# Kernel tuning notes

Hardware: AMD Instinct MI355X
Metric: run time of the kernel (lower is better)

The kernel has to match this reference:

```python
import jax, jax.numpy as jnp
import numpy as np

D_MODEL = 768
NUM_HEADS = 12
HEAD_DIM = D_MODEL // NUM_HEADS
LN_EPS = 1e-5
MASK_NEG = -1000000.0


def setup_inputs() -> dict:
    key = jax.random.key(0)
    ks = jax.random.split(key, 10)
    B, L, S = 2, 2048, 2048
    s = 1.0 / np.sqrt(D_MODEL)
    return {
        "q": jax.random.normal(ks[0], (B, L, D_MODEL), jnp.float32),
        "k": jax.random.normal(ks[1], (B, S, D_MODEL), jnp.float32),
        "v": jax.random.normal(ks[2], (B, S, D_MODEL), jnp.float32),
        "attention_mask": jnp.ones((B, S), jnp.int32),
        "Wq": jax.random.normal(ks[3], (D_MODEL, D_MODEL), jnp.float32) * s,
        "Wk": jax.random.normal(ks[4], (D_MODEL, D_MODEL), jnp.float32) * s,
        "Wv": jax.random.normal(ks[5], (D_MODEL, D_MODEL), jnp.float32) * s,
        "W": jax.random.normal(ks[6], (D_MODEL, D_MODEL), jnp.float32) * s,
        "b": jnp.zeros((D_MODEL,), jnp.float32),
        "gamma": jnp.ones((D_MODEL,), jnp.float32),
        "beta": jnp.zeros((D_MODEL,), jnp.float32),
    }


def reference(q, k, v, attention_mask, Wq, Wk, Wv, W, b, gamma, beta):
    B, L, D = q.shape
    S = k.shape[1]
    H, hd = NUM_HEADS, HEAD_DIM
    # projections (torch Linear: x @ W^T), split heads -> (B,H,L,hd)
    Q = (q @ Wq.T).reshape(B, L, H, hd).transpose(0, 2, 1, 3)
    K = (k @ Wk.T).reshape(B, S, H, hd).transpose(0, 2, 1, 3)
    V = (v @ Wv.T).reshape(B, S, H, hd).transpose(0, 2, 1, 3)
    # scores (B,H,L,S) with additive key-padding mask
    scores = jnp.einsum("bhld,bhsd->bhls", Q, K) / np.sqrt(hd)
    mask_score = (1.0 - attention_mask.astype(q.dtype))[:, None, None, :] * MASK_NEG
    att = jax.nn.softmax(scores + mask_score, axis=-1)  # dropout p=0 (eval)
    # attend, merge heads, output projection (with bias)
    O = jnp.einsum("bhls,bhsd->bhld", att, V).transpose(0, 2, 1, 3).reshape(B, L, D)
    O = O @ W.T + b  # state dropout p=0 (eval)
    # residual + LayerNorm
    x = q + O
    mu = jnp.mean(x, axis=-1, keepdims=True)
    var = jnp.mean(jnp.square(x - mu), axis=-1, keepdims=True)
    return (x - mu) * jax.lax.rsqrt(var + LN_EPS) * gamma + beta
```

## Files before the change

kernel.cpp:

```cpp
#include <hip/hip_runtime.h>
#include <hip/hip_bf16.h>
#include <math.h>


typedef unsigned short u16;
typedef unsigned int   u32;
typedef __bf16 bf16x8 __attribute__((ext_vector_type(8)));
typedef float  f32x4  __attribute__((ext_vector_type(4)));

#define DM   768
#define MR   4096
#define WSZ  589824

#define LOG2E 1.44269504089f
#define SM_C  15.0f
#define K1    (0.125f * LOG2E)

__device__ inline u16 bfbits(float f) {
    union { __bf16 b; u16 u; } x; x.b = (__bf16)f; return x.u;
}

__device__ inline uint4 cvt8(const float* src) {
    const float4* p = reinterpret_cast<const float4*>(src);
    float4 a = p[0], b = p[1];
    union { __bf16 h[8]; uint4 v; } u;
    u.h[0] = (__bf16)a.x; u.h[1] = (__bf16)a.y; u.h[2] = (__bf16)a.z; u.h[3] = (__bf16)a.w;
    u.h[4] = (__bf16)b.x; u.h[5] = (__bf16)b.y; u.h[6] = (__bf16)b.z; u.h[7] = (__bf16)b.w;
    return u.v;
}

__device__ inline uint4 cvt8v(float4 a, float4 b) {
    union { __bf16 h[8]; uint4 v; } u;
    u.h[0] = (__bf16)a.x; u.h[1] = (__bf16)a.y; u.h[2] = (__bf16)a.z; u.h[3] = (__bf16)a.w;
    u.h[4] = (__bf16)b.x; u.h[5] = (__bf16)b.y; u.h[6] = (__bf16)b.z; u.h[7] = (__bf16)b.w;
    return u.v;
}

__global__ __launch_bounds__(256) void wcvt(
    const float* __restrict__ w0, const float* __restrict__ w1,
    const float* __restrict__ w2, const float* __restrict__ w3,
    u16* __restrict__ dst)
{
    const float* src = (blockIdx.y == 0) ? w0 : (blockIdx.y == 1) ? w1
                     : (blockIdx.y == 2) ? w2 : w3;
    size_t idx = ((size_t)blockIdx.x * 256 + threadIdx.x) * 8;
    *reinterpret_cast<uint4*>(&dst[(size_t)blockIdx.y * WSZ + idx]) = cvt8(&src[idx]);
}

__global__ __launch_bounds__(256, 2) void gemm_qkv(
    const float* __restrict__ xq, const float* __restrict__ xk, const float* __restrict__ xv,
    const u16* __restrict__ Wb4,
    u16* __restrict__ oq, u16* __restrict__ ok, u16* __restrict__ ov)
{
    const int mode = blockIdx.z;
    const float* X = (mode == 0) ? xq : (mode == 1) ? xk : xv;
    const u16* Wb  = Wb4 + (size_t)mode * WSZ;
    u16* out       = (mode == 0) ? oq : (mode == 1) ? ok : ov;

    __shared__ __attribute__((aligned(16))) u16 As[2][64][72];
    __shared__ __attribute__((aligned(16))) u16 Bs[2][64][72];

    const int tid  = threadIdx.x;
    const int lane = tid & 63;
    const int w    = tid >> 6;
    const int wm   = (w >> 1) * 32;
    const int wn   = (w & 1) * 32;
    const int quad = lane >> 4;
    const int l16  = lane & 15;
    const int tm   = blockIdx.x * 64;
    const int tn   = blockIdx.y * 64;

    const int row0 = tid >> 3,         col0 = (tid & 7) * 8;
    const int row1 = (tid + 256) >> 3, col1 = ((tid + 256) & 7) * 8;

    const float* a0p = &X[(size_t)(tm + row0) * 768 + col0];
    const float* a1p = &X[(size_t)(tm + row1) * 768 + col1];
    const u16*   b0p = &Wb[(size_t)(tn + row0) * 768 + col0];
    const u16*   b1p = &Wb[(size_t)(tn + row1) * 768 + col1];

    f32x4 acc[2][2] = {};

    {
        *reinterpret_cast<uint4*>(&As[0][row0][col0]) = cvt8(a0p);
        *reinterpret_cast<uint4*>(&As[0][row1][col1]) = cvt8(a1p);
        *reinterpret_cast<uint4*>(&Bs[0][row0][col0]) = *reinterpret_cast<const uint4*>(b0p);
        *reinterpret_cast<uint4*>(&Bs[0][row1][col1]) = *reinterpret_cast<const uint4*>(b1p);
    }

    for (int kt = 0; kt < 12; kt++) {
        const int cur = kt & 1;
        __syncthreads();

        float4 af0a, af0b, af1a, af1b; uint4 bt0, bt1;
        if (kt < 11) {
            const int ko = (kt + 1) * 64;
            af0a = *reinterpret_cast<const float4*>(a0p + ko);
            af0b = *reinterpret_cast<const float4*>(a0p + ko + 4);
            af1a = *reinterpret_cast<const float4*>(a1p + ko);
            af1b = *reinterpret_cast<const float4*>(a1p + ko + 4);
            bt0  = *reinterpret_cast<const uint4*>(b0p + ko);
            bt1  = *reinterpret_cast<const uint4*>(b1p + ko);
        }

        #pragma unroll
        for (int kk = 0; kk < 2; kk++) {
            bf16x8 a0 = *reinterpret_cast<const bf16x8*>(&As[cur][wm + l16     ][kk*32 + quad*8]);
            bf16x8 a1 = *reinterpret_cast<const bf16x8*>(&As[cur][wm + 16 + l16][kk*32 + quad*8]);
            bf16x8 b0 = *reinterpret_cast<const bf16x8*>(&Bs[cur][wn + l16     ][kk*32 + quad*8]);
            bf16x8 b1 = *reinterpret_cast<const bf16x8*>(&Bs[cur][wn + 16 + l16][kk*32 + quad*8]);
            acc[0][0] = __builtin_amdgcn_mfma_f32_16x16x32_bf16(a0, b0, acc[0][0], 0, 0, 0);
            acc[0][1] = __builtin_amdgcn_mfma_f32_16x16x32_bf16(a0, b1, acc[0][1], 0, 0, 0);
            acc[1][0] = __builtin_amdgcn_mfma_f32_16x16x32_bf16(a1, b0, acc[1][0], 0, 0, 0);
            acc[1][1] = __builtin_amdgcn_mfma_f32_16x16x32_bf16(a1, b1, acc[1][1], 0, 0, 0);
        }

        if (kt < 11) {
            const int nxt = cur ^ 1;
            *reinterpret_cast<uint4*>(&As[nxt][row0][col0]) = cvt8v(af0a, af0b);
            *reinterpret_cast<uint4*>(&As[nxt][row1][col1]) = cvt8v(af1a, af1b);
            *reinterpret_cast<uint4*>(&Bs[nxt][row0][col0]) = bt0;
            *reinterpret_cast<uint4*>(&Bs[nxt][row1][col1]) = bt1;
        }
    }

    #pragma unroll
    for (int i = 0; i < 2; i++)
        #pragma unroll
        for (int j = 0; j < 2; j++)
            #pragma unroll
            for (int r = 0; r < 4; r++) {
                int gm = tm + wm + i * 16 + quad * 4 + r;
                int gn = tn + wn + j * 16 + l16;
                int b = gm >> 11, l = gm & 2047;
                int h = gn >> 6,  d = gn & 63;
                u16 bv = bfbits(acc[i][j][r]);
                if (mode == 2)
                    out[((size_t)(b * 12 + h) * 64 + d) * 2048 + l] = bv;
                else
                    out[((size_t)(b * 12 + h) * 2048 + l) * 64 + d] = bv;
            }
}

__global__ __launch_bounds__(256, 2) void gemm_out(
    const u16* __restrict__ Oa, const u16* __restrict__ Wb,
    const float* __restrict__ bias, const float* __restrict__ resid,
    float* __restrict__ Xb)
{
    __shared__ __attribute__((aligned(16))) u16 As[2][64][72];
    __shared__ __attribute__((aligned(16))) u16 Bs[2][64][72];

    const int tid  = threadIdx.x;
    const int lane = tid & 63;
    const int w    = tid >> 6;
    const int wm   = (w >> 1) * 32;
    const int wn   = (w & 1) * 32;
    const int quad = lane >> 4;
    const int l16  = lane & 15;
    const int tm   = blockIdx.x * 64;
    const int tn   = blockIdx.y * 64;

    const int row0 = tid >> 3,         col0 = (tid & 7) * 8;
    const int row1 = (tid + 256) >> 3, col1 = ((tid + 256) & 7) * 8;

    const u16* a0p = &Oa[(size_t)(tm + row0) * 768 + col0];
    const u16* a1p = &Oa[(size_t)(tm + row1) * 768 + col1];
    const u16* b0p = &Wb[(size_t)(tn + row0) * 768 + col0];
    const u16* b1p = &Wb[(size_t)(tn + row1) * 768 + col1];

    f32x4 acc[2][2] = {};

    {
        *reinterpret_cast<uint4*>(&As[0][row0][col0]) = *reinterpret_cast<const uint4*>(a0p);
        *reinterpret_cast<uint4*>(&As[0][row1][col1]) = *reinterpret_cast<const uint4*>(a1p);
        *reinterpret_cast<uint4*>(&Bs[0][row0][col0]) = *reinterpret_cast<const uint4*>(b0p);
        *reinterpret_cast<uint4*>(&Bs[0][row1][col1]) = *reinterpret_cast<const uint4*>(b1p);
    }

    for (int kt = 0; kt < 12; kt++) {
        const int cur = kt & 1;
        __syncthreads();

        uint4 at0, at1, bt0, bt1;
        if (kt < 11) {
            const int ko = (kt + 1) * 64;
            at0 = *reinterpret_cast<const uint4*>(a0p + ko);
            at1 = *reinterpret_cast<const uint4*>(a1p + ko);
            bt0 = *reinterpret_cast<const uint4*>(b0p + ko);
            bt1 = *reinterpret_cast<const uint4*>(b1p + ko);
        }

        #pragma unroll
        for (int kk = 0; kk < 2; kk++) {
            bf16x8 a0 = *reinterpret_cast<const bf16x8*>(&As[cur][wm + l16     ][kk*32 + quad*8]);
            bf16x8 a1 = *reinterpret_cast<const bf16x8*>(&As[cur][wm + 16 + l16][kk*32 + quad*8]);
            bf16x8 b0 = *reinterpret_cast<const bf16x8*>(&Bs[cur][wn + l16     ][kk*32 + quad*8]);
            bf16x8 b1 = *reinterpret_cast<const bf16x8*>(&Bs[cur][wn + 16 + l16][kk*32 + quad*8]);
            acc[0][0] = __builtin_amdgcn_mfma_f32_16x16x32_bf16(a0, b0, acc[0][0], 0, 0, 0);
            acc[0][1] = __builtin_amdgcn_mfma_f32_16x16x32_bf16(a0, b1, acc[0][1], 0, 0, 0);
            acc[1][0] = __builtin_amdgcn_mfma_f32_16x16x32_bf16(a1, b0, acc[1][0], 0, 0, 0);
            acc[1][1] = __builtin_amdgcn_mfma_f32_16x16x32_bf16(a1, b1, acc[1][1], 0, 0, 0);
        }

        if (kt < 11) {
            const int nxt = cur ^ 1;
            *reinterpret_cast<uint4*>(&As[nxt][row0][col0]) = at0;
            *reinterpret_cast<uint4*>(&As[nxt][row1][col1]) = at1;
            *reinterpret_cast<uint4*>(&Bs[nxt][row0][col0]) = bt0;
            *reinterpret_cast<uint4*>(&Bs[nxt][row1][col1]) = bt1;
        }
    }

    #pragma unroll
    for (int i = 0; i < 2; i++)
        #pragma unroll
        for (int j = 0; j < 2; j++)
            #pragma unroll
            for (int r = 0; r < 4; r++) {
                int gm = tm + wm + i * 16 + quad * 4 + r;
                int gn = tn + wn + j * 16 + l16;
                Xb[(size_t)gm * 768 + gn] = acc[i][j][r] + bias[gn] + resid[(size_t)gm * 768 + gn];
            }
}

__global__ __launch_bounds__(256, 3) void attn(
    const u16* __restrict__ Qp, const u16* __restrict__ Kp, const u16* __restrict__ Vt,
    const int* __restrict__ amask, u16* __restrict__ Oatt)
{
    __shared__ __attribute__((aligned(16))) unsigned char smem[4 * 64 * 40 * 2 + 2048 * 4];
    u16 (*Ps)[64][40] = reinterpret_cast<u16(*)[64][40]>(smem);
    float* maskC = reinterpret_cast<float*>(smem + 20480);
    float (*Obuf)[68] = reinterpret_cast<float(*)[68]>(smem);

    const int tid  = threadIdx.x;
    const int lane = tid & 63;
    const int w    = tid >> 6;
    const int quad = lane >> 4;
    const int l16  = lane & 15;
    const int qt = blockIdx.x;
    const int h  = blockIdx.y;
    const int b  = blockIdx.z;

    #pragma unroll
    for (int i = 0; i < 8; i++) {
        int s = tid + i * 256;
        maskC[s] = amask[b * 2048 + s] ? (-SM_C * LOG2E) : -2.0e6f;
    }
    __syncthreads();

    const u16* Qbase = Qp + ((size_t)(b * 12 + h) * 2048 + qt * 64) * 64;
    const u16* Kb2   = Kp + (size_t)(b * 12 + h) * 2048 * 64 + (size_t)w * 32 * 64;
    const u16* Vb2   = Vt + (size_t)(b * 12 + h) * 64 * 2048 + (size_t)w * 32;

    bf16x8 qfrag[4][2];
    #pragma unroll
    for (int qb = 0; qb < 4; qb++)
        #pragma unroll
        for (int kk = 0; kk < 2; kk++)
            qfrag[qb][kk] = *reinterpret_cast<const bf16x8*>(
                &Qbase[(qb * 16 + l16) * 64 + kk * 32 + quad * 8]);

    bf16x8 onesf = {};
    if (l16 == 0) {
        #pragma unroll
        for (int i = 0; i < 8; i++) onesf[i] = (__bf16)1.0f;
    }

    f32x4 oacc[4][4] = {};
    f32x4 sacc[4]    = {};

    for (int st = 0; st < 16; st++) {
        bf16x8 kf[2][2], vf[4];
        #pragma unroll
        for (int ct = 0; ct < 2; ct++)
            #pragma unroll
            for (int kk = 0; kk < 2; kk++)
                kf[ct][kk] = *reinterpret_cast<const bf16x8*>(
                    &Kb2[(size_t)(st * 128 + ct * 16 + l16) * 64 + kk * 32 + quad * 8]);
        #pragma unroll
        for (int cd = 0; cd < 4; cd++)
            vf[cd] = *reinterpret_cast<const bf16x8*>(
                &Vb2[(size_t)(cd * 16 + l16) * 2048 + st * 128 + quad * 8]);

        #pragma unroll
        for (int qb = 0; qb < 4; qb++)
            #pragma unroll
            for (int ct = 0; ct < 2; ct++) {
                f32x4 s = {};
                __builtin_amdgcn_s_setprio(1);
                s = __builtin_amdgcn_mfma_f32_16x16x32_bf16(kf[ct][0], qfrag[qb][0], s, 0, 0, 0);
                s = __builtin_amdgcn_mfma_f32_16x16x32_bf16(kf[ct][1], qfrag[qb][1], s, 0, 0, 0);
                __builtin_amdgcn_s_setprio(0);
                f32x4 cc = *reinterpret_cast<const f32x4*>(
                    &maskC[st * 128 + w * 32 + ct * 16 + quad * 4]);
                union { u16 h[4]; uint2 v2; } pk;
                #pragma unroll
                for (int r = 0; r < 4; r++)
                    pk.h[r] = bfbits(__builtin_amdgcn_exp2f(__builtin_fmaf(s[r], K1, cc[r])));
                *reinterpret_cast<uint2*>(&Ps[w][qb * 16 + l16][ct * 16 + quad * 4]) = pk.v2;
            }

        bf16x8 pf[4];
        #pragma unroll
        for (int qb = 0; qb < 4; qb++)
            pf[qb] = *reinterpret_cast<const bf16x8*>(&Ps[w][qb * 16 + l16][quad * 8]);
        __builtin_amdgcn_s_setprio(1);
        #pragma unroll
        for (int qb = 0; qb < 4; qb++)
            sacc[qb] = __builtin_amdgcn_mfma_f32_16x16x32_bf16(pf[qb], onesf, sacc[qb], 0, 0, 0);
        #pragma unroll
        for (int qb = 0; qb < 4; qb++)
            #pragma unroll
            for (int cd = 0; cd < 4; cd++)
                oacc[qb][cd] = __builtin_amdgcn_mfma_f32_16x16x32_bf16(pf[qb], vf[cd], oacc[qb][cd], 0, 0, 0);
        __builtin_amdgcn_s_setprio(0);
    }

    __syncthreads();
    for (int wv = 0; wv < 4; wv++) {
        if (w == wv) {
            #pragma unroll
            for (int qb = 0; qb < 4; qb++) {
                #pragma unroll
                for (int cd = 0; cd < 4; cd++)
                    #pragma unroll
                    for (int r = 0; r < 4; r++) {
                        float* cell = &Obuf[qb * 16 + quad * 4 + r][cd * 16 + l16];
                        if (wv == 0) *cell = oacc[qb][cd][r];
                        else         *cell += oacc[qb][cd][r];
                    }
                if (l16 == 0) {
                    #pragma unroll
                    for (int r = 0; r < 4; r++) {
                        float* cell = &Obuf[qb * 16 + quad * 4 + r][64];
                        if (wv == 0) *cell = sacc[qb][r];
                        else         *cell += sacc[qb][r];
                    }
                }
            }
        }
        __syncthreads();
    }

    #pragma unroll
    for (int g = 0; g < 4; g++) {
        int unit = tid + g * 256;
        int row = unit >> 4;
        int c4  = (unit & 15) * 4;
        float rinv = 1.0f / Obuf[row][64];
        union { u16 h[4]; uint2 v; } o;
        #pragma unroll
        for (int j = 0; j < 4; j++)
            o.h[j] = bfbits(Obuf[row][c4 + j] * rinv);
        *reinterpret_cast<uint2*>(
            &Oatt[(size_t)(b * 2048 + qt * 64 + row) * 768 + h * 64 + c4]) = o.v;
    }
}

__global__ __launch_bounds__(256) void ln_kernel(
    float* __restrict__ X, const float* __restrict__ gamma,
    const float* __restrict__ beta)
{
    const int tid  = threadIdx.x;
    const int w    = tid >> 6;
    const int lane = tid & 63;
    const int row  = blockIdx.x * 4 + w;
    float* xr = X + (size_t)row * 768;

    float4 v[3];
    float s = 0.f, s2 = 0.f;
    #pragma unroll
    for (int i = 0; i < 3; i++) {
        v[i] = *reinterpret_cast<const float4*>(&xr[i * 256 + lane * 4]);
        s  += v[i].x + v[i].y + v[i].z + v[i].w;
        s2 += v[i].x * v[i].x + v[i].y * v[i].y + v[i].z * v[i].z + v[i].w * v[i].w;
    }
    #pragma unroll
    for (int off = 32; off >= 1; off >>= 1) {
        s  += __shfl_xor(s,  off, 64);
        s2 += __shfl_xor(s2, off, 64);
    }
    float mu  = s * (1.0f / 768.0f);
    float var = s2 * (1.0f / 768.0f) - mu * mu;
    float rstd = rsqrtf(var + 1e-5f);
    #pragma unroll
    for (int i = 0; i < 3; i++) {
        int c = i * 256 + lane * 4;
        float4 g  = *reinterpret_cast<const float4*>(&gamma[c]);
        float4 bt = *reinterpret_cast<const float4*>(&beta[c]);
        float4 o;
        o.x = (v[i].x - mu) * rstd * g.x + bt.x;
        o.y = (v[i].y - mu) * rstd * g.y + bt.y;
        o.z = (v[i].z - mu) * rstd * g.z + bt.z;
        o.w = (v[i].w - mu) * rstd * g.w + bt.w;
        *reinterpret_cast<float4*>(&xr[c]) = o;
    }
}

extern "C" void kernel_launch(void* const* d_in, const int* in_sizes, int n_in,
                              void* d_out, int out_size, void* d_ws, size_t ws_size,
                              hipStream_t stream)
{
    const float* q   = (const float*)d_in[0];
    const float* k   = (const float*)d_in[1];
    const float* v   = (const float*)d_in[2];
    const int*   am  = (const int*)d_in[3];
    const float* Wq  = (const float*)d_in[4];
    const float* Wk  = (const float*)d_in[5];
    const float* Wv  = (const float*)d_in[6];
    const float* W   = (const float*)d_in[7];
    const float* bb  = (const float*)d_in[8];
    const float* gam = (const float*)d_in[9];
    const float* bet = (const float*)d_in[10];

    u16* Wb4 = (u16*)d_ws;
    u16* Qp  = Wb4 + (size_t)4 * WSZ;
    u16* Kp  = Qp + (size_t)MR * DM;
    u16* Vt  = Kp + (size_t)MR * DM;
    u16* Oa  = Vt + (size_t)MR * DM;
    float* Xb = (float*)d_out;

    wcvt<<<dim3(288, 4), 256, 0, stream>>>(Wq, Wk, Wv, W, Wb4);
    gemm_qkv<<<dim3(64, 12, 3), 256, 0, stream>>>(q, k, v, Wb4, Qp, Kp, Vt);
    attn<<<dim3(32, 12, 2), 256, 0, stream>>>(Qp, Kp, Vt, am, Oa);
    gemm_out<<<dim3(64, 12), 256, 0, stream>>>(Oa, Wb4 + (size_t)3 * WSZ, bb, q, Xb);
    ln_kernel<<<1024, 256, 0, stream>>>(Xb, gam, bet);
}
```

Baseline: 218.1 us.

## Precompute mask in wcvt, single-buffer GEMM B tiles, drop attention setprio

The attention mask constants are now computed once by an extra block column in the weight-conversion kernel and written to a global float buffer. Attention reads them straight from global memory instead of building a per-block LDS copy, which frees 8 KB of LDS per block and removes a barrier. Both GEMMs keep the weight tile in a single LDS buffer held in registers across iterations, at the cost of an extra barrier per k-step. The s_setprio hints around the attention MFMAs are also removed.

```diff
diff --git a/kernel.cpp b/kernel.cpp
--- a/kernel.cpp
+++ b/kernel.cpp
@@ -39,8 +39,20 @@
 __global__ __launch_bounds__(256) void wcvt(
     const float* __restrict__ w0, const float* __restrict__ w1,
     const float* __restrict__ w2, const float* __restrict__ w3,
-    u16* __restrict__ dst)
-{
+    const int* __restrict__ am, u16* __restrict__ dst,
+    float* __restrict__ maskF)
+{
+    if (blockIdx.x == 288) {
+        int i = (blockIdx.y * 256 + threadIdx.x) * 4;
+        int4 m = *reinterpret_cast<const int4*>(&am[i]);
+        float4 o;
+        o.x = m.x ? (-SM_C * LOG2E) : -2.0e6f;
+        o.y = m.y ? (-SM_C * LOG2E) : -2.0e6f;
+        o.z = m.z ? (-SM_C * LOG2E) : -2.0e6f;
+        o.w = m.w ? (-SM_C * LOG2E) : -2.0e6f;
+        *reinterpret_cast<float4*>(&maskF[i]) = o;
+        return;
+    }
     const float* src = (blockIdx.y == 0) ? w0 : (blockIdx.y == 1) ? w1
                      : (blockIdx.y == 2) ? w2 : w3;
     size_t idx = ((size_t)blockIdx.x * 256 + threadIdx.x) * 8;
@@ -58,7 +70,7 @@
     u16* out       = (mode == 0) ? oq : (mode == 1) ? ok : ov;
 
     __shared__ __attribute__((aligned(16))) u16 As[2][64][72];
-    __shared__ __attribute__((aligned(16))) u16 Bs[2][64][72];
+    __shared__ __attribute__((aligned(16))) u16 Bs[64][72];
 
     const int tid  = threadIdx.x;
     const int lane = tid & 63;
@@ -80,18 +92,19 @@
 
     f32x4 acc[2][2] = {};
 
-    {
-        *reinterpret_cast<uint4*>(&As[0][row0][col0]) = cvt8(a0p);
-        *reinterpret_cast<uint4*>(&As[0][row1][col1]) = cvt8(a1p);
-        *reinterpret_cast<uint4*>(&Bs[0][row0][col0]) = *reinterpret_cast<const uint4*>(b0p);
-        *reinterpret_cast<uint4*>(&Bs[0][row1][col1]) = *reinterpret_cast<const uint4*>(b1p);
-    }
+    *reinterpret_cast<uint4*>(&As[0][row0][col0]) = cvt8(a0p);
+    *reinterpret_cast<uint4*>(&As[0][row1][col1]) = cvt8(a1p);
+    uint4 bt0 = *reinterpret_cast<const uint4*>(b0p);
+    uint4 bt1 = *reinterpret_cast<const uint4*>(b1p);
 
     for (int kt = 0; kt < 12; kt++) {
         const int cur = kt & 1;
+        if (kt) __syncthreads();
+        *reinterpret_cast<uint4*>(&Bs[row0][col0]) = bt0;
+        *reinterpret_cast<uint4*>(&Bs[row1][col1]) = bt1;
         __syncthreads();
 
-        float4 af0a, af0b, af1a, af1b; uint4 bt0, bt1;
+        float4 af0a, af0b, af1a, af1b;
         if (kt < 11) {
             const int ko = (kt + 1) * 64;
             af0a = *reinterpret_cast<const float4*>(a0p + ko);
@@ -106,8 +119,8 @@
         for (int kk = 0; kk < 2; kk++) {
             bf16x8 a0 = *reinterpret_cast<const bf16x8*>(&As[cur][wm + l16     ][kk*32 + quad*8]);
             bf16x8 a1 = *reinterpret_cast<const bf16x8*>(&As[cur][wm + 16 + l16][kk*32 + quad*8]);
-            bf16x8 b0 = *reinterpret_cast<const bf16x8*>(&Bs[cur][wn + l16     ][kk*32 + quad*8]);
-            bf16x8 b1 = *reinterpret_cast<const bf16x8*>(&Bs[cur][wn + 16 + l16][kk*32 + quad*8]);
+            bf16x8 b0 = *reinterpret_cast<const bf16x8*>(&Bs[wn + l16     ][kk*32 + quad*8]);
+            bf16x8 b1 = *reinterpret_cast<const bf16x8*>(&Bs[wn + 16 + l16][kk*32 + quad*8]);
             acc[0][0] = __builtin_amdgcn_mfma_f32_16x16x32_bf16(a0, b0, acc[0][0], 0, 0, 0);
             acc[0][1] = __builtin_amdgcn_mfma_f32_16x16x32_bf16(a0, b1, acc[0][1], 0, 0, 0);
             acc[1][0] = __builtin_amdgcn_mfma_f32_16x16x32_bf16(a1, b0, acc[1][0], 0, 0, 0);
@@ -118,8 +131,6 @@
             const int nxt = cur ^ 1;
             *reinterpret_cast<uint4*>(&As[nxt][row0][col0]) = cvt8v(af0a, af0b);
             *reinterpret_cast<uint4*>(&As[nxt][row1][col1]) = cvt8v(af1a, af1b);
-            *reinterpret_cast<uint4*>(&Bs[nxt][row0][col0]) = bt0;
-            *reinterpret_cast<uint4*>(&Bs[nxt][row1][col1]) = bt1;
         }
     }
 
@@ -147,7 +158,7 @@
     float* __restrict__ Xb)
 {
     __shared__ __attribute__((aligned(16))) u16 As[2][64][72];
-    __shared__ __attribute__((aligned(16))) u16 Bs[2][64][72];
+    __shared__ __attribute__((aligned(16))) u16 Bs[64][72];
 
     const int tid  = threadIdx.x;
     const int lane = tid & 63;
@@ -169,18 +180,19 @@
 
     f32x4 acc[2][2] = {};
 
-    {
-        *reinterpret_cast<uint4*>(&As[0][row0][col0]) = *reinterpret_cast<const uint4*>(a0p);
-        *reinterpret_cast<uint4*>(&As[0][row1][col1]) = *reinterpret_cast<const uint4*>(a1p);
-        *reinterpret_cast<uint4*>(&Bs[0][row0][col0]) = *reinterpret_cast<const uint4*>(b0p);
-        *reinterpret_cast<uint4*>(&Bs[0][row1][col1]) = *reinterpret_cast<const uint4*>(b1p);
-    }
+    *reinterpret_cast<uint4*>(&As[0][row0][col0]) = *reinterpret_cast<const uint4*>(a0p);
+    *reinterpret_cast<uint4*>(&As[0][row1][col1]) = *reinterpret_cast<const uint4*>(a1p);
+    uint4 bt0 = *reinterpret_cast<const uint4*>(b0p);
+    uint4 bt1 = *reinterpret_cast<const uint4*>(b1p);
 
     for (int kt = 0; kt < 12; kt++) {
         const int cur = kt & 1;
+        if (kt) __syncthreads();
+        *reinterpret_cast<uint4*>(&Bs[row0][col0]) = bt0;
+        *reinterpret_cast<uint4*>(&Bs[row1][col1]) = bt1;
         __syncthreads();
 
-        uint4 at0, at1, bt0, bt1;
+        uint4 at0, at1;
         if (kt < 11) {
             const int ko = (kt + 1) * 64;
             at0 = *reinterpret_cast<const uint4*>(a0p + ko);
@@ -193,8 +205,8 @@
         for (int kk = 0; kk < 2; kk++) {
             bf16x8 a0 = *reinterpret_cast<const bf16x8*>(&As[cur][wm + l16     ][kk*32 + quad*8]);
             bf16x8 a1 = *reinterpret_cast<const bf16x8*>(&As[cur][wm + 16 + l16][kk*32 + quad*8]);
-            bf16x8 b0 = *reinterpret_cast<const bf16x8*>(&Bs[cur][wn + l16     ][kk*32 + quad*8]);
-            bf16x8 b1 = *reinterpret_cast<const bf16x8*>(&Bs[cur][wn + 16 + l16][kk*32 + quad*8]);
+            bf16x8 b0 = *reinterpret_cast<const bf16x8*>(&Bs[wn + l16     ][kk*32 + quad*8]);
+            bf16x8 b1 = *reinterpret_cast<const bf16x8*>(&Bs[wn + 16 + l16][kk*32 + quad*8]);
             acc[0][0] = __builtin_amdgcn_mfma_f32_16x16x32_bf16(a0, b0, acc[0][0], 0, 0, 0);
             acc[0][1] = __builtin_amdgcn_mfma_f32_16x16x32_bf16(a0, b1, acc[0][1], 0, 0, 0);
             acc[1][0] = __builtin_amdgcn_mfma_f32_16x16x32_bf16(a1, b0, acc[1][0], 0, 0, 0);
@@ -205,8 +217,6 @@
             const int nxt = cur ^ 1;
             *reinterpret_cast<uint4*>(&As[nxt][row0][col0]) = at0;
             *reinterpret_cast<uint4*>(&As[nxt][row1][col1]) = at1;
-            *reinterpret_cast<uint4*>(&Bs[nxt][row0][col0]) = bt0;
-            *reinterpret_cast<uint4*>(&Bs[nxt][row1][col1]) = bt1;
         }
     }
 
@@ -224,11 +234,10 @@
 
 __global__ __launch_bounds__(256, 3) void attn(
     const u16* __restrict__ Qp, const u16* __restrict__ Kp, const u16* __restrict__ Vt,
-    const int* __restrict__ amask, u16* __restrict__ Oatt)
-{
-    __shared__ __attribute__((aligned(16))) unsigned char smem[4 * 64 * 40 * 2 + 2048 * 4];
+    const float* __restrict__ maskF, u16* __restrict__ Oatt)
+{
+    __shared__ __attribute__((aligned(16))) unsigned char smem[4 * 64 * 40 * 2];
     u16 (*Ps)[64][40] = reinterpret_cast<u16(*)[64][40]>(smem);
-    float* maskC = reinterpret_cast<float*>(smem + 20480);
     float (*Obuf)[68] = reinterpret_cast<float(*)[68]>(smem);
 
     const int tid  = threadIdx.x;
@@ -240,16 +249,10 @@
     const int h  = blockIdx.y;
     const int b  = blockIdx.z;
 
-    #pragma unroll
-    for (int i = 0; i < 8; i++) {
-        int s = tid + i * 256;
-        maskC[s] = amask[b * 2048 + s] ? (-SM_C * LOG2E) : -2.0e6f;
-    }
-    __syncthreads();
-
     const u16* Qbase = Qp + ((size_t)(b * 12 + h) * 2048 + qt * 64) * 64;
     const u16* Kb2   = Kp + (size_t)(b * 12 + h) * 2048 * 64 + (size_t)w * 32 * 64;
     const u16* Vb2   = Vt + (size_t)(b * 12 + h) * 64 * 2048 + (size_t)w * 32;
+    const float* mB  = maskF + b * 2048 + w * 32;
 
     bf16x8 qfrag[4][2];
     #pragma unroll
@@ -286,12 +289,10 @@
             #pragma unroll
             for (int ct = 0; ct < 2; ct++) {
                 f32x4 s = {};
-                __builtin_amdgcn_s_setprio(1);
                 s = __builtin_amdgcn_mfma_f32_16x16x32_bf16(kf[ct][0], qfrag[qb][0], s, 0, 0, 0);
                 s = __builtin_amdgcn_mfma_f32_16x16x32_bf16(kf[ct][1], qfrag[qb][1], s, 0, 0, 0);
-                __builtin_amdgcn_s_setprio(0);
                 f32x4 cc = *reinterpret_cast<const f32x4*>(
-                    &maskC[st * 128 + w * 32 + ct * 16 + quad * 4]);
+                    &mB[st * 128 + ct * 16 + quad * 4]);
                 union { u16 h[4]; uint2 v2; } pk;
                 #pragma unroll
                 for (int r = 0; r < 4; r++)
@@ -303,7 +304,6 @@
         #pragma unroll
         for (int qb = 0; qb < 4; qb++)
             pf[qb] = *reinterpret_cast<const bf16x8*>(&Ps[w][qb * 16 + l16][quad * 8]);
-        __builtin_amdgcn_s_setprio(1);
         #pragma unroll
         for (int qb = 0; qb < 4; qb++)
             sacc[qb] = __builtin_amdgcn_mfma_f32_16x16x32_bf16(pf[qb], onesf, sacc[qb], 0, 0, 0);
@@ -312,7 +312,6 @@
             #pragma unroll
             for (int cd = 0; cd < 4; cd++)
                 oacc[qb][cd] = __builtin_amdgcn_mfma_f32_16x16x32_bf16(pf[qb], vf[cd], oacc[qb][cd], 0, 0, 0);
-        __builtin_amdgcn_s_setprio(0);
     }
 
     __syncthreads();
@@ -417,11 +416,12 @@
     u16* Kp  = Qp + (size_t)MR * DM;
     u16* Vt  = Kp + (size_t)MR * DM;
     u16* Oa  = Vt + (size_t)MR * DM;
+    float* maskF = (float*)(Oa + (size_t)MR * DM);
     float* Xb = (float*)d_out;
 
-    wcvt<<<dim3(288, 4), 256, 0, stream>>>(Wq, Wk, Wv, W, Wb4);
+    wcvt<<<dim3(289, 4), 256, 0, stream>>>(Wq, Wk, Wv, W, am, Wb4, maskF);
     gemm_qkv<<<dim3(64, 12, 3), 256, 0, stream>>>(q, k, v, Wb4, Qp, Kp, Vt);
-    attn<<<dim3(32, 12, 2), 256, 0, stream>>>(Qp, Kp, Vt, am, Oa);
+    attn<<<dim3(32, 12, 2), 256, 0, stream>>>(Qp, Kp, Vt, maskF, Oa);
     gemm_out<<<dim3(64, 12), 256, 0, stream>>>(Oa, Wb4 + (size_t)3 * WSZ, bb, q, Xb);
     ln_kernel<<<1024, 256, 0, stream>>>(Xb, gam, bet);
 }
```

New measurement: 228.8 us. +4.9%, slower.
